# Performance work log

Measured on AMD Instinct MI355X. Metric: run time of the kernel, lower is better.

Reference implementation:

```python
import jax, jax.numpy as jnp
import numpy as np

B, N, H = 32, 512, 128
LN_EPS = 1e-5

def _layernorm(x):
    # LayerNorm over last dim, no affine (elementwise_affine=False)
    mu = jnp.mean(x, axis=-1, keepdims=True)
    var = jnp.var(x, axis=-1, keepdims=True)
    return (x - mu) * jax.lax.rsqrt(var + LN_EPS)

def setup_inputs() -> dict:
    key = jax.random.key(0)
    k0, k1, k2, k3 = jax.random.split(key, 4)
    s = jax.random.normal(k0, (B, N, H), dtype=jnp.float32)
    ev = jax.random.normal(k1, (B, N, N, 3), dtype=jnp.float32)
    mask = (jax.random.uniform(k2, (B, N, N, 1)) > 0.5).astype(jnp.float32)
    W1 = jax.random.normal(k3, (H, H), dtype=jnp.float32) / np.sqrt(H)
    b1 = jnp.zeros((H,), dtype=jnp.float32)
    return {"s": s, "ev": ev, "mask": mask, "W1": W1, "b1": b1}

def reference(s, ev, mask, W1, b1):
    # lin1: Linear -> LayerNorm (no affine) -> SiLU
    h = jnp.einsum('bnh,kh->bnk', s, W1) + b1          # (B, N, H)
    h = jax.nn.silu(_layernorm(h))
    # Fused CFConv: v[b,i,c,d] = sum_j mask[b,i,j] * ev[b,i,j,c] * h[b,j,d]
    mev = ev * mask                                     # (B, N, N, 3)
    v = jnp.einsum('bijc,bjd->bicd', mev, h)            # (B, N, 3, H)
    return v
```

## Files before the change

kernel.cpp:

```cpp
#include <hip/hip_runtime.h>
#include <hip/hip_bf16.h>

#define B_ 32
#define N_ 512
#define H_ 128

typedef float f32x4 __attribute__((ext_vector_type(4)));
typedef short short8 __attribute__((ext_vector_type(8)));
typedef short short4v __attribute__((ext_vector_type(4)));

static __device__ __forceinline__ float bf2f(unsigned short u) {
  union { unsigned int ui; float f; } x;
  x.ui = ((unsigned int)u) << 16;
  return x.f;
}
static __device__ __forceinline__ unsigned short f2bf(float f) {
  __hip_bfloat16 h = __float2bfloat16(f);
  return *reinterpret_cast<unsigned short*>(&h);
}

__global__ __launch_bounds__(256) void lin_ln_silu_kernel(
    const float* __restrict__ s, const float* __restrict__ W1,
    const float* __restrict__ b1, unsigned short* __restrict__ h_t) {
  __shared__ float s_sh[32 * 132];
  __shared__ unsigned short w_sh[128 * 132];
  __shared__ unsigned short ht_sh[128 * 40];
  const int t = threadIdx.x;
  const int b = blockIdx.y;
  const int n0 = blockIdx.x * 32;

#pragma unroll
  for (int r = 0; r < 16; ++r) {
    int q = t + 256 * r;
    int d = q >> 5, part = q & 31;
    float4 v = *reinterpret_cast<const float4*>(W1 + d * H_ + part * 4);
    short4v w;
    w.x = (short)f2bf(v.x); w.y = (short)f2bf(v.y);
    w.z = (short)f2bf(v.z); w.w = (short)f2bf(v.w);
    *reinterpret_cast<short4v*>(&w_sh[d * 132 + part * 4]) = w;
  }
#pragma unroll
  for (int r = 0; r < 4; ++r) {
    int q = t + 256 * r;
    int n = q >> 5, part = q & 31;
    float4 v = *reinterpret_cast<const float4*>(
        s + ((size_t)b * N_ + n0 + n) * H_ + part * 4);
    *reinterpret_cast<float4*>(&s_sh[n * 132 + part * 4]) = v;
  }
  __syncthreads();

  const int a = t & 15;
  const int g = t >> 4;
  float acc[2][8];
#pragma unroll
  for (int nn = 0; nn < 2; ++nn)
#pragma unroll
    for (int dd = 0; dd < 8; ++dd) acc[nn][dd] = 0.f;

  float bias[8];
#pragma unroll
  for (int dd = 0; dd < 8; ++dd) bias[dd] = b1[dd * 16 + a];

  for (int k = 0; k < 128; k += 4) {
    float wf[8][4];
#pragma unroll
    for (int dd = 0; dd < 8; ++dd) {
      short4v wv =
          *reinterpret_cast<const short4v*>(&w_sh[(dd * 16 + a) * 132 + k]);
      wf[dd][0] = bf2f((unsigned short)wv.x);
      wf[dd][1] = bf2f((unsigned short)wv.y);
      wf[dd][2] = bf2f((unsigned short)wv.z);
      wf[dd][3] = bf2f((unsigned short)wv.w);
    }
#pragma unroll
    for (int nn = 0; nn < 2; ++nn) {
      float4 sv =
          *reinterpret_cast<const float4*>(&s_sh[(nn * 16 + g) * 132 + k]);
#pragma unroll
      for (int dd = 0; dd < 8; ++dd) {
        acc[nn][dd] += sv.x * wf[dd][0] + sv.y * wf[dd][1] +
                       sv.z * wf[dd][2] + sv.w * wf[dd][3];
      }
    }
  }

#pragma unroll
  for (int nn = 0; nn < 2; ++nn) {
    float s1 = 0.f, s2 = 0.f;
#pragma unroll
    for (int dd = 0; dd < 8; ++dd) {
      float x = acc[nn][dd] + bias[dd];
      acc[nn][dd] = x;
      s1 += x;
      s2 += x * x;
    }
#pragma unroll
    for (int off = 8; off >= 1; off >>= 1) {
      s1 += __shfl_xor(s1, off);
      s2 += __shfl_xor(s2, off);
    }
    float mean = s1 * (1.f / 128.f);
    float var = s2 * (1.f / 128.f) - mean * mean;
    float rs = rsqrtf(var + 1e-5f);
#pragma unroll
    for (int dd = 0; dd < 8; ++dd) {
      float x = (acc[nn][dd] - mean) * rs;
      float y = x / (1.f + __expf(-x));
      ht_sh[(dd * 16 + a) * 40 + nn * 16 + g] = f2bf(y);
    }
  }
  __syncthreads();

#pragma unroll
  for (int r = 0; r < 2; ++r) {
    int q = t + 256 * r;
    int d = q >> 2, part = q & 3;
    float4 v = *reinterpret_cast<const float4*>(&ht_sh[d * 40 + part * 8]);
    *reinterpret_cast<float4*>(
        h_t + ((size_t)b * 128 + d) * 512 + n0 + part * 8) = v;
  }
}

__global__ __launch_bounds__(256) void cfconv_mfma_kernel(
    const float* __restrict__ ev, const float* __restrict__ mask,
    const unsigned short* __restrict__ h_t, float* __restrict__ out) {
  __shared__ unsigned short ph[48 * 72];
  __shared__ unsigned short hh[128 * 72];
  const int t = threadIdx.x;
  const int b = blockIdx.y;
  const int i0 = blockIdx.x * 16;
  const int lane = t & 63;
  const int w = t >> 6;
  const int l15 = lane & 15;
  const int quad = lane >> 4;

  f32x4 acc[3][2];
#pragma unroll
  for (int mt = 0; mt < 3; ++mt)
#pragma unroll
    for (int nt = 0; nt < 2; ++nt)
#pragma unroll
      for (int e = 0; e < 4; ++e) acc[mt][nt][e] = 0.f;

  for (int j0 = 0; j0 < N_; j0 += 64) {
    __syncthreads();

#pragma unroll
    for (int r = 0; r < 4; ++r) {
      int q = t + 256 * r;
      int d = q >> 3, p8 = q & 7;
      float4 v = *reinterpret_cast<const float4*>(
          h_t + ((size_t)b * 128 + d) * 512 + j0 + p8 * 8);
      *reinterpret_cast<float4*>(&hh[d * 72 + p8 * 8]) = v;
    }

#pragma unroll
    for (int r = 0; r < 3; ++r) {
      int q = t + 256 * r;
      int i = q / 48, part = q % 48;
      int f0 = part * 4;
      const float* evbase =
          ev + ((size_t)((b * N_ + i0 + i)) * N_ + j0) * 3;
      float4 e4 = *reinterpret_cast<const float4*>(evbase + f0);
      const float* mrow = mask + (size_t)(b * N_ + i0 + i) * N_ + j0;
      int jlo = f0 / 3, jhi = (f0 + 3) / 3;
      float mlo = mrow[jlo], mhi = mrow[jhi];
      float evv[4] = {e4.x, e4.y, e4.z, e4.w};
#pragma unroll
      for (int e = 0; e < 4; ++e) {
        int f = f0 + e;
        int j = f / 3, c = f - 3 * j;
        float m = (j == jlo) ? mlo : mhi;
        ph[(c * 16 + i) * 72 + j] = f2bf(evv[e] * m);
      }
    }
    __syncthreads();

#pragma unroll
    for (int ks = 0; ks < 2; ++ks) {
      short8 av[3], bv[2];
#pragma unroll
      for (int mt = 0; mt < 3; ++mt)
        av[mt] = *reinterpret_cast<const short8*>(
            &ph[(mt * 16 + l15) * 72 + ks * 32 + quad * 8]);
#pragma unroll
      for (int nt = 0; nt < 2; ++nt) {
        int d = w * 32 + nt * 16 + l15;
        bv[nt] = *reinterpret_cast<const short8*>(
            &hh[d * 72 + ks * 32 + quad * 8]);
      }
#pragma unroll
      for (int mt = 0; mt < 3; ++mt)
#pragma unroll
        for (int nt = 0; nt < 2; ++nt)
          acc[mt][nt] = __builtin_amdgcn_mfma_f32_16x16x32_bf16(
              av[mt], bv[nt], acc[mt][nt], 0, 0, 0);
    }
  }

#pragma unroll
  for (int mt = 0; mt < 3; ++mt) {
#pragma unroll
    for (int nt = 0; nt < 2; ++nt) {
      int d = w * 32 + nt * 16 + l15;
#pragma unroll
      for (int r = 0; r < 4; ++r) {
        int i = i0 + quad * 4 + r;
        out[(((size_t)b * N_ + i) * 3 + mt) * H_ + d] = acc[mt][nt][r];
      }
    }
  }
}

extern "C" void kernel_launch(void* const* d_in, const int* in_sizes, int n_in,
                              void* d_out, int out_size, void* d_ws,
                              size_t ws_size, hipStream_t stream) {
  const float* s = (const float*)d_in[0];
  const float* ev = (const float*)d_in[1];
  const float* mask = (const float*)d_in[2];
  const float* W1 = (const float*)d_in[3];
  const float* b1 = (const float*)d_in[4];
  float* out = (float*)d_out;
  unsigned short* h_t = (unsigned short*)d_ws;

  lin_ln_silu_kernel<<<dim3(N_ / 32, B_), 256, 0, stream>>>(s, W1, b1, h_t);
  cfconv_mfma_kernel<<<dim3(N_ / 16, B_), 256, 0, stream>>>(ev, mask, h_t, out);
}
```

Baseline: 214.1 us.

## Use MFMA for linear layer and drop LDS staging in CFConv kernel

The first kernel's scalar FMA GEMM becomes 16x16x32 bf16 MFMA on single-wavefront blocks that load s and W1 straight from global memory. The CFConv kernel now runs one wavefront per block and splits H into two 64-wide halves across the grid. Each lane loads ev, mask and h_t directly into registers and builds the MFMA fragments itself, with no shared memory and no barriers. This removes the LDS round trips and syncs, but ev and mask are now read twice (once per H half) and global loads are less coalesced.

```diff
diff --git a/kernel.cpp b/kernel.cpp
--- a/kernel.cpp
+++ b/kernel.cpp
@@ -7,90 +7,67 @@
 
 typedef float f32x4 __attribute__((ext_vector_type(4)));
 typedef short short8 __attribute__((ext_vector_type(8)));
-typedef short short4v __attribute__((ext_vector_type(4)));
 
-static __device__ __forceinline__ float bf2f(unsigned short u) {
-  union { unsigned int ui; float f; } x;
-  x.ui = ((unsigned int)u) << 16;
-  return x.f;
-}
 static __device__ __forceinline__ unsigned short f2bf(float f) {
   __hip_bfloat16 h = __float2bfloat16(f);
   return *reinterpret_cast<unsigned short*>(&h);
 }
+static __device__ __forceinline__ short8 pack8(float a0, float a1, float a2,
+                                               float a3, float a4, float a5,
+                                               float a6, float a7) {
+  short8 v;
+  v[0] = (short)f2bf(a0); v[1] = (short)f2bf(a1);
+  v[2] = (short)f2bf(a2); v[3] = (short)f2bf(a3);
+  v[4] = (short)f2bf(a4); v[5] = (short)f2bf(a5);
+  v[6] = (short)f2bf(a6); v[7] = (short)f2bf(a7);
+  return v;
+}
 
-__global__ __launch_bounds__(256) void lin_ln_silu_kernel(
+__global__ __launch_bounds__(64) void lin_ln_silu_kernel(
     const float* __restrict__ s, const float* __restrict__ W1,
     const float* __restrict__ b1, unsigned short* __restrict__ h_t) {
-  __shared__ float s_sh[32 * 132];
-  __shared__ unsigned short w_sh[128 * 132];
-  __shared__ unsigned short ht_sh[128 * 40];
+  __shared__ unsigned short trans[128 * 16];
   const int t = threadIdx.x;
+  const int n0 = blockIdx.x * 16;
   const int b = blockIdx.y;
-  const int n0 = blockIdx.x * 32;
+  const int l15 = t & 15;
+  const int quad = t >> 4;
+
+  f32x4 acc[8];
+#pragma unroll
+  for (int nt = 0; nt < 8; ++nt)
+#pragma unroll
+    for (int e = 0; e < 4; ++e) acc[nt][e] = 0.f;
+
+  const float* srow = s + ((size_t)b * N_ + n0 + l15) * H_;
 
 #pragma unroll
-  for (int r = 0; r < 16; ++r) {
-    int q = t + 256 * r;
-    int d = q >> 5, part = q & 31;
-    float4 v = *reinterpret_cast<const float4*>(W1 + d * H_ + part * 4);
-    short4v w;
-    w.x = (short)f2bf(v.x); w.y = (short)f2bf(v.y);
-    w.z = (short)f2bf(v.z); w.w = (short)f2bf(v.w);
-    *reinterpret_cast<short4v*>(&w_sh[d * 132 + part * 4]) = w;
-  }
+  for (int ks = 0; ks < 4; ++ks) {
+    const int k = ks * 32 + quad * 8;
+    float4 a0 = *reinterpret_cast<const float4*>(srow + k);
+    float4 a1 = *reinterpret_cast<const float4*>(srow + k + 4);
+    short8 av = pack8(a0.x, a0.y, a0.z, a0.w, a1.x, a1.y, a1.z, a1.w);
 #pragma unroll
-  for (int r = 0; r < 4; ++r) {
-    int q = t + 256 * r;
-    int n = q >> 5, part = q & 31;
-    float4 v = *reinterpret_cast<const float4*>(
-        s + ((size_t)b * N_ + n0 + n) * H_ + part * 4);
-    *reinterpret_cast<float4*>(&s_sh[n * 132 + part * 4]) = v;
-  }
-  __syncthreads();
-
-  const int a = t & 15;
-  const int g = t >> 4;
-  float acc[2][8];
-#pragma unroll
-  for (int nn = 0; nn < 2; ++nn)
-#pragma unroll
-    for (int dd = 0; dd < 8; ++dd) acc[nn][dd] = 0.f;
-
-  float bias[8];
-#pragma unroll
-  for (int dd = 0; dd < 8; ++dd) bias[dd] = b1[dd * 16 + a];
-
-  for (int k = 0; k < 128; k += 4) {
-    float wf[8][4];
-#pragma unroll
-    for (int dd = 0; dd < 8; ++dd) {
-      short4v wv =
-          *reinterpret_cast<const short4v*>(&w_sh[(dd * 16 + a) * 132 + k]);
-      wf[dd][0] = bf2f((unsigned short)wv.x);
-      wf[dd][1] = bf2f((unsigned short)wv.y);
-      wf[dd][2] = bf2f((unsigned short)wv.z);
-      wf[dd][3] = bf2f((unsigned short)wv.w);
-    }
-#pragma unroll
-    for (int nn = 0; nn < 2; ++nn) {
-      float4 sv =
-          *reinterpret_cast<const float4*>(&s_sh[(nn * 16 + g) * 132 + k]);
-#pragma unroll
-      for (int dd = 0; dd < 8; ++dd) {
-        acc[nn][dd] += sv.x * wf[dd][0] + sv.y * wf[dd][1] +
-                       sv.z * wf[dd][2] + sv.w * wf[dd][3];
-      }
+    for (int nt = 0; nt < 8; ++nt) {
+      const float* wrow = W1 + (size_t)(nt * 16 + l15) * H_ + k;
+      float4 w0 = *reinterpret_cast<const float4*>(wrow);
+      float4 w1 = *reinterpret_cast<const float4*>(wrow + 4);
+      short8 bv = pack8(w0.x, w0.y, w0.z, w0.w, w1.x, w1.y, w1.z, w1.w);
+      acc[nt] = __builtin_amdgcn_mfma_f32_16x16x32_bf16(av, bv, acc[nt], 0, 0, 0);
     }
   }
 
+  float bb[8];
 #pragma unroll
-  for (int nn = 0; nn < 2; ++nn) {
+  for (int nt = 0; nt < 8; ++nt) bb[nt] = b1[nt * 16 + l15];
+
+#pragma unroll
+  for (int r = 0; r < 4; ++r) {
     float s1 = 0.f, s2 = 0.f;
 #pragma unroll
-    for (int dd = 0; dd < 8; ++dd) {
-      float x = acc[nn][dd] + bias[dd];
-      acc[nn][dd] = x;
+    for (int nt = 0; nt < 8; ++nt) {
+      float x = acc[nt][r] + bb[nt];
+      acc[nt][r] = x;
       s1 += x;
       s2 += x * x;
     }
@@ -103,113 +80,102 @@
     float var = s2 * (1.f / 128.f) - mean * mean;
     float rs = rsqrtf(var + 1e-5f);
 #pragma unroll
-    for (int dd = 0; dd < 8; ++dd) {
-      float x = (acc[nn][dd] - mean) * rs;
+    for (int nt = 0; nt < 8; ++nt) {
+      float x = (acc[nt][r] - mean) * rs;
       float y = x / (1.f + __expf(-x));
-      ht_sh[(dd * 16 + a) * 40 + nn * 16 + g] = f2bf(y);
+      trans[(nt * 16 + l15) * 16 + quad * 4 + r] = f2bf(y);
     }
   }
   __syncthreads();
 
 #pragma unroll
-  for (int r = 0; r < 2; ++r) {
-    int q = t + 256 * r;
-    int d = q >> 2, part = q & 3;
-    float4 v = *reinterpret_cast<const float4*>(&ht_sh[d * 40 + part * 8]);
-    *reinterpret_cast<float4*>(
-        h_t + ((size_t)b * 128 + d) * 512 + n0 + part * 8) = v;
+  for (int r2 = 0; r2 < 2; ++r2) {
+    int d = t + 64 * r2;
+    unsigned short* dst = h_t + ((size_t)b * H_ + d) * N_ + n0;
+    short8 v0 = *reinterpret_cast<const short8*>(&trans[d * 16]);
+    short8 v1 = *reinterpret_cast<const short8*>(&trans[d * 16 + 8]);
+    *reinterpret_cast<short8*>(dst) = v0;
+    *reinterpret_cast<short8*>(dst + 8) = v1;
   }
 }
 
-__global__ __launch_bounds__(256) void cfconv_mfma_kernel(
+__global__ __launch_bounds__(64, 2) void cfconv_mfma_kernel(
     const float* __restrict__ ev, const float* __restrict__ mask,
     const unsigned short* __restrict__ h_t, float* __restrict__ out) {
-  __shared__ unsigned short ph[48 * 72];
-  __shared__ unsigned short hh[128 * 72];
   const int t = threadIdx.x;
-  const int b = blockIdx.y;
   const int i0 = blockIdx.x * 16;
-  const int lane = t & 63;
-  const int w = t >> 6;
-  const int l15 = lane & 15;
-  const int quad = lane >> 4;
+  const int dh = blockIdx.y * 64;
+  const int b = blockIdx.z;
+  const int l15 = t & 15;
+  const int quad = t >> 4;
 
-  f32x4 acc[3][2];
+  const float* evrow = ev + ((size_t)(b * N_ + i0 + l15) * N_) * 3;
+  const float* mrow = mask + (size_t)(b * N_ + i0 + l15) * N_;
+  const unsigned short* hrow = h_t + ((size_t)b * H_ + dh) * N_;
+
+  f32x4 acc[3][4];
 #pragma unroll
-  for (int mt = 0; mt < 3; ++mt)
+  for (int c = 0; c < 3; ++c)
 #pragma unroll
-    for (int nt = 0; nt < 2; ++nt)
+    for (int nt = 0; nt < 4; ++nt)
 #pragma unroll
-      for (int e = 0; e < 4; ++e) acc[mt][nt][e] = 0.f;
-
-  for (int j0 = 0; j0 < N_; j0 += 64) {
-    __syncthreads();
+      for (int e = 0; e < 4; ++e) acc[c][nt][e] = 0.f;
 
 #pragma unroll
-    for (int r = 0; r < 4; ++r) {
-      int q = t + 256 * r;
-      int d = q >> 3, p8 = q & 7;
-      float4 v = *reinterpret_cast<const float4*>(
-          h_t + ((size_t)b * 128 + d) * 512 + j0 + p8 * 8);
-      *reinterpret_cast<float4*>(&hh[d * 72 + p8 * 8]) = v;
-    }
+  for (int sl = 0; sl < 16; ++sl) {
+    const int j0 = sl * 32 + quad * 8;
+
+    float4 e0 = *reinterpret_cast<const float4*>(evrow + j0 * 3);
+    float4 e1 = *reinterpret_cast<const float4*>(evrow + j0 * 3 + 4);
+    float4 e2 = *reinterpret_cast<const float4*>(evrow + j0 * 3 + 8);
+    float4 e3 = *reinterpret_cast<const float4*>(evrow + j0 * 3 + 12);
+    float4 e4 = *reinterpret_cast<const float4*>(evrow + j0 * 3 + 16);
+    float4 e5 = *reinterpret_cast<const float4*>(evrow + j0 * 3 + 20);
+    float4 m0 = *reinterpret_cast<const float4*>(mrow + j0);
+    float4 m1 = *reinterpret_cast<const float4*>(mrow + j0 + 4);
+
+    short8 bv[4];
+#pragma unroll
+    for (int nt = 0; nt < 4; ++nt)
+      bv[nt] = *reinterpret_cast<const short8*>(
+          hrow + (size_t)(nt * 16 + l15) * N_ + j0);
+
+    const float f0 = e0.x, f1 = e0.y, f2 = e0.z, f3 = e0.w;
+    const float f4 = e1.x, f5 = e1.y, f6 = e1.z, f7 = e1.w;
+    const float f8 = e2.x, f9 = e2.y, f10 = e2.z, f11 = e2.w;
+    const float f12 = e3.x, f13 = e3.y, f14 = e3.z, f15 = e3.w;
+    const float f16 = e4.x, f17 = e4.y, f18 = e4.z, f19 = e4.w;
+    const float f20 = e5.x, f21 = e5.y, f22 = e5.z, f23 = e5.w;
+    const float k0 = m0.x, k1 = m0.y, k2 = m0.z, k3 = m0.w;
+    const float k4 = m1.x, k5 = m1.y, k6 = m1.z, k7 = m1.w;
+
+    short8 av[3];
+    av[0] = pack8(f0 * k0, f3 * k1, f6 * k2, f9 * k3, f12 * k4, f15 * k5,
+                  f18 * k6, f21 * k7);
+    av[1] = pack8(f1 * k0, f4 * k1, f7 * k2, f10 * k3, f13 * k4, f16 * k5,
+                  f19 * k6, f22 * k7);
+    av[2] = pack8(f2 * k0, f5 * k1, f8 * k2, f11 * k3, f14 * k4, f17 * k5,
+                  f20 * k6, f23 * k7);
 
 #pragma unroll
-    for (int r = 0; r < 3; ++r) {
-      int q = t + 256 * r;
-      int i = q / 48, part = q % 48;
-      int f0 = part * 4;
-      const float* evbase =
-          ev + ((size_t)((b * N_ + i0 + i)) * N_ + j0) * 3;
-      float4 e4 = *reinterpret_cast<const float4*>(evbase + f0);
-      const float* mrow = mask + (size_t)(b * N_ + i0 + i) * N_ + j0;
-      int jlo = f0 / 3, jhi = (f0 + 3) / 3;
-      float mlo = mrow[jlo], mhi = mrow[jhi];
-      float evv[4] = {e4.x, e4.y, e4.z, e4.w};
+    for (int c = 0; c < 3; ++c)
 #pragma unroll
-      for (int e = 0; e < 4; ++e) {
-        int f = f0 + e;
-        int j = f / 3, c = f - 3 * j;
-        float m = (j == jlo) ? mlo : mhi;
-        ph[(c * 16 + i) * 72 + j] = f2bf(evv[e] * m);
-      }
-    }
-    __syncthreads();
-
-#pragma unroll
-    for (int ks = 0; ks < 2; ++ks) {
-      short8 av[3], bv[2];
-#pragma unroll
-      for (int mt = 0; mt < 3; ++mt)
-        av[mt] = *reinterpret_cast<const short8*>(
-            &ph[(mt * 16 + l15) * 72 + ks * 32 + quad * 8]);
-#pragma unroll
-      for (int nt = 0; nt < 2; ++nt) {
-        int d = w * 32 + nt * 16 + l15;
-        bv[nt] = *reinterpret_cast<const short8*>(
-            &hh[d * 72 + ks * 32 + quad * 8]);
-      }
-#pragma unroll
-      for (int mt = 0; mt < 3; ++mt)
-#pragma unroll
-        for (int nt = 0; nt < 2; ++nt)
-          acc[mt][nt] = __builtin_amdgcn_mfma_f32_16x16x32_bf16(
-              av[mt], bv[nt], acc[mt][nt], 0, 0, 0);
-    }
+      for (int nt = 0; nt < 4; ++nt)
+        acc[c][nt] = __builtin_amdgcn_mfma_f32_16x16x32_bf16(av[c], bv[nt],
+                                                             acc[c][nt], 0, 0, 0);
   }
 
 #pragma unroll
-  for (int mt = 0; mt < 3; ++mt) {
+  for (int c = 0; c < 3; ++c)
 #pragma unroll
-    for (int nt = 0; nt < 2; ++nt) {
-      int d = w * 32 + nt * 16 + l15;
+    for (int nt = 0; nt < 4; ++nt) {
+      const int d = dh + nt * 16 + l15;
 #pragma unroll
       for (int r = 0; r < 4; ++r) {
-        int i = i0 + quad * 4 + r;
-        out[(((size_t)b * N_ + i) * 3 + mt) * H_ + d] = acc[mt][nt][r];
+        const int i = i0 + quad * 4 + r;
+        out[(((size_t)b * N_ + i) * 3 + c) * H_ + d] = acc[c][nt][r];
       }
     }
-  }
 }
 
 extern "C" void kernel_launch(void* const* d_in, const int* in_sizes, int n_in,
@@ -223,6 +189,7 @@
   float* out = (float*)d_out;
   unsigned short* h_t = (unsigned short*)d_ws;
 
-  lin_ln_silu_kernel<<<dim3(N_ / 32, B_), 256, 0, stream>>>(s, W1, b1, h_t);
-  cfconv_mfma_kernel<<<dim3(N_ / 16, B_), 256, 0, stream>>>(ev, mask, h_t, out);
+  lin_ln_silu_kernel<<<dim3(N_ / 16, B_), 64, 0, stream>>>(s, W1, b1, h_t);
+  cfconv_mfma_kernel<<<dim3(N_ / 16, 2, B_), 64, 0, stream>>>(ev, mask, h_t,
+                                                              out);
 }
```

Result: slower. 229.3 us (+7.1%).
